# Performance work log

Hardware: AMD Instinct MI355X
Metric: run time of the kernel (lower is better)

Reference implementation:

```python
import jax, jax.numpy as jnp
import numpy as np

N_NODES = 131072
N_EDGES = 1048576
N_GRAPHS = 1024
EMB = 96
HID = 64
OUT = 3
NEG_SLOPE = 0.2  # PyG GATConv default leaky_relu slope


def setup_inputs() -> dict:
    key = jax.random.key(0)
    ks = jax.random.split(key, 8)
    x = jax.random.normal(ks[0], (N_NODES, EMB), dtype=jnp.float32)
    edge_index = jax.random.randint(ks[1], (2, N_EDGES), 0, N_NODES, dtype=jnp.int64)
    batch = jnp.sort(jax.random.randint(ks[2], (N_NODES,), 0, N_GRAPHS, dtype=jnp.int64))
    s = 1.0 / np.sqrt(EMB)
    W = jax.random.uniform(ks[3], (EMB, HID), jnp.float32, -s, s)       # GATConv lin (no bias)
    att_src = jax.random.uniform(ks[4], (HID,), jnp.float32, -s, s)     # a_src
    att_dst = jax.random.uniform(ks[5], (HID,), jnp.float32, -s, s)     # a_dst
    bias_gat = jnp.zeros((HID,), jnp.float32)
    sf = 1.0 / np.sqrt(HID)
    fc_w = jax.random.uniform(ks[6], (OUT, HID), jnp.float32, -sf, sf)
    fc_b = jax.random.uniform(ks[7], (OUT,), jnp.float32, -sf, sf)
    return {"x": x, "edge_index": edge_index, "batch": batch, "W": W,
            "att_src": att_src, "att_dst": att_dst, "bias_gat": bias_gat,
            "fc_w": fc_w, "fc_b": fc_b}


def _segment_softmax(logits, seg, num_segments):
    # numerically stable softmax over edges grouped by target node
    m = jax.ops.segment_max(logits, seg, num_segments=num_segments)
    e = jnp.exp(logits - m[seg])
    z = jax.ops.segment_sum(e, seg, num_segments=num_segments)
    return e / (z[seg] + 1e-16)


def reference(x, edge_index, batch, W, att_src, att_dst, bias_gat, fc_w, fc_b):
    N = x.shape[0]
    # PyG GATConv (heads=1): add self loops
    loop = jnp.arange(N, dtype=edge_index.dtype)
    src = jnp.concatenate([edge_index[0], loop])
    dst = jnp.concatenate([edge_index[1], loop])

    h = x @ W                                    # [N, HID]
    a_s = h @ att_src                            # [N]
    a_d = h @ att_dst                            # [N]
    logits = jax.nn.leaky_relu(a_s[src] + a_d[dst], NEG_SLOPE)  # [E]
    alpha = _segment_softmax(logits, dst, N)     # softmax over in-edges per target
    out = jax.ops.segment_sum(alpha[:, None] * h[src], dst, num_segments=N)
    out = out + bias_gat                         # [N, HID]

    # global_mean_pool over graphs
    sums = jax.ops.segment_sum(out, batch, num_segments=N_GRAPHS)
    cnt = jax.ops.segment_sum(jnp.ones((N,), out.dtype), batch, num_segments=N_GRAPHS)
    pooled = sums / jnp.maximum(cnt, 1.0)[:, None]  # [G, HID]

    logits_out = pooled @ fc_w.T + fc_b          # [G, OUT]
    return jax.nn.log_softmax(logits_out, axis=1)
```

## Files before the change

### kernel.cpp

```cpp
#include <hip/hip_runtime.h>
#include <hip/hip_fp16.h>

#define N_NODES 131072
#define N_EDGES 1048576
#define N_GRAPHS 1024
#define EMB 96
#define HID 64
#define CAP 32
#define NBKT 128
#define NCHUNK 1024
#define BCAP2 32

typedef _Float16 half8 __attribute__((ext_vector_type(8)));
typedef float float4v __attribute__((ext_vector_type(4)));

__global__ __launch_bounds__(256) void k_bucket(const int* __restrict__ src,
    const int* __restrict__ dst, int* __restrict__ ebuf, int* __restrict__ ccnt,
    const float* __restrict__ W, _Float16* __restrict__ Wt)
{
    int tid = threadIdx.x;
    int blk = blockIdx.x;
    __shared__ int bcnt[NBKT];
    if (tid < NBKT) bcnt[tid] = 0;
    if (blk < 24) {
        int t = blk * 256 + tid;
        Wt[(t & 63) * EMB + (t >> 6)] = (_Float16)W[t];
    }
    __syncthreads();
    int e0 = blk * 1024;
    #pragma unroll
    for (int i = 0; i < 4; ++i) {
        int e = e0 + i * 256 + tid;
        int sv = src[e], dv = dst[e];
        int b = dv >> 10;
        int r = atomicAdd(&bcnt[b], 1);
        if (r < BCAP2)
            ebuf[((size_t)b * NCHUNK + blk) * BCAP2 + r] = (sv << 10) | (dv & 1023);
    }
    __syncthreads();
    if (tid < NBKT) {
        int v = bcnt[tid];
        ccnt[tid * NCHUNK + blk] = v < BCAP2 ? v : BCAP2;
    }
}

__global__ __launch_bounds__(512, 4) void k_lin_place(
    const float* __restrict__ x, const _Float16* __restrict__ Wt,
    const float* __restrict__ att_src, const float* __restrict__ att_dst,
    __half* __restrict__ h, float* __restrict__ a_s, float* __restrict__ a_d,
    const int* __restrict__ ebuf, const int* __restrict__ ccnt,
    int* __restrict__ cnt, int* __restrict__ slots,
    float* __restrict__ pool, float* __restrict__ gcnt)
{
    int tid = threadIdx.x;
    __shared__ int cl[1024];
    __shared__ int cm[1024];

    if (blockIdx.x < NBKT) {
        int b = blockIdx.x;
        cl[tid] = 0; cl[tid + 512] = 0;
        cm[tid] = ccnt[b * NCHUNK + tid];
        cm[tid + 512] = ccnt[b * NCHUNK + 512 + tid];
        pool[b * 512 + tid] = 0.f;
        if (b == 0) { gcnt[tid] = 0.f; gcnt[tid + 512] = 0.f; }
        __syncthreads();
        int lane = tid & 63;
        int w = tid >> 6;
        int half = lane >> 5;
        int s32 = lane & 31;
        const int* eb = ebuf + (size_t)b * NCHUNK * BCAP2;
        int bbase = b << 10;
        for (int it0 = 0; it0 < 64; it0 += 8) {
            int e[8];
            #pragma unroll
            for (int k = 0; k < 8; ++k) {
                int c = w * 128 + (it0 + k) * 2 + half;
                e[k] = eb[c * BCAP2 + s32];
            }
            #pragma unroll
            for (int k = 0; k < 8; ++k) {
                int c = w * 128 + (it0 + k) * 2 + half;
                if (s32 < cm[c]) {
                    int local = e[k] & 1023;
                    int slot = atomicAdd(&cl[local], 1);
                    if (slot < CAP)
                        slots[(size_t)(bbase | local) * CAP + slot] = e[k] >> 10;
                }
            }
        }
        __syncthreads();
        cnt[b * 1024 + tid] = cl[tid];
        cnt[b * 1024 + 512 + tid] = cl[tid + 512];
    } else {
        int sub = blockIdx.x - NBKT;
        int lane = tid & 63;
        int w = tid >> 6;
        int m16 = lane & 15;
        int quad = lane >> 4;
        int rowbase = sub * 128 + w * 16;

        half8 bf[4][3];
        #pragma unroll
        for (int nt = 0; nt < 4; ++nt)
            #pragma unroll
            for (int kb = 0; kb < 3; ++kb)
                bf[nt][kb] = *(const half8*)(Wt + (nt * 16 + m16) * EMB
                                             + kb * 32 + quad * 8);

        float4v acc[4];
        #pragma unroll
        for (int nt = 0; nt < 4; ++nt)
            acc[nt] = (float4v){0.f, 0.f, 0.f, 0.f};

        const float* xrow = x + (size_t)(rowbase + m16) * EMB + quad * 8;
        #pragma unroll
        for (int kb = 0; kb < 3; ++kb) {
            float4 xa = *(const float4*)(xrow + kb * 32);
            float4 xb = *(const float4*)(xrow + kb * 32 + 4);
            half8 af;
            af[0] = (_Float16)xa.x; af[1] = (_Float16)xa.y;
            af[2] = (_Float16)xa.z; af[3] = (_Float16)xa.w;
            af[4] = (_Float16)xb.x; af[5] = (_Float16)xb.y;
            af[6] = (_Float16)xb.z; af[7] = (_Float16)xb.w;
            #pragma unroll
            for (int nt = 0; nt < 4; ++nt)
                acc[nt] = __builtin_amdgcn_mfma_f32_16x16x32_f16(
                    af, bf[nt][kb], acc[nt], 0, 0, 0);
        }

        float asv[4], adv[4];
        #pragma unroll
        for (int nt = 0; nt < 4; ++nt) {
            asv[nt] = att_src[nt * 16 + m16];
            adv[nt] = att_dst[nt * 16 + m16];
        }

        #pragma unroll
        for (int r = 0; r < 4; ++r) {
            int row = rowbase + quad * 4 + r;
            float ps = 0.f, pd = 0.f;
            #pragma unroll
            for (int nt = 0; nt < 4; ++nt) {
                float v = acc[nt][r];
                h[(size_t)row * HID + nt * 16 + m16] = __float2half(v);
                ps += v * asv[nt];
                pd += v * adv[nt];
            }
            #pragma unroll
            for (int off = 8; off >= 1; off >>= 1) {
                ps += __shfl_xor(ps, off, 64);
                pd += __shfl_xor(pd, off, 64);
            }
            if (m16 == 0) { a_s[row] = ps; a_d[row] = pd; }
        }
    }
}

__global__ __launch_bounds__(256, 6) void k_accum(const __half2* __restrict__ h2,
    const float* __restrict__ a_s, const float* __restrict__ a_d,
    const int* __restrict__ cnt, const int* __restrict__ slots,
    const float* __restrict__ bias, __half2* __restrict__ out)
{
    int tid = threadIdx.x;
    int lane = tid & 63;
    int sub = lane & 31;
    int gbase = lane & 32;
    int node = blockIdx.x * 8 + ((tid >> 6) << 1) + (gbase >> 5);

    int deg = cnt[node]; if (deg > CAP) deg = CAP;
    int s_j = node;
    if (sub < deg) s_j = slots[(size_t)node * CAP + sub];

    __half2 hv = h2[(size_t)node * 32 + sub];
    __half2 hg[16];
    #pragma unroll
    for (int k = 0; k < 16; ++k) {
        int i = __shfl(s_j, gbase + k, 64);
        hg[k] = h2[(size_t)i * 32 + sub];
    }
    float asg = a_s[s_j];
    float adi = a_d[node];
    float asi = a_s[node];

    float t = asg + adi;
    t = t > 0.f ? t : 0.2f * t;
    float w_j = (sub < deg) ? __expf(t) : 0.f;

    float t0 = asi + adi;
    t0 = t0 > 0.f ? t0 : 0.2f * t0;
    float w0 = __expf(t0);

    float z = w_j;
    #pragma unroll
    for (int off = 16; off >= 1; off >>= 1) z += __shfl_xor(z, off, 64);
    z += w0;

    float2 acc;
    acc.x = w0 * __half2float(hv.x);
    acc.y = w0 * __half2float(hv.y);
    #pragma unroll
    for (int k = 0; k < 16; ++k) {
        float wk = __shfl(w_j, gbase + k, 64);
        acc.x += wk * __half2float(hg[k].x);
        acc.y += wk * __half2float(hg[k].y);
    }

    for (int j0 = 16; j0 < deg; j0 += 8) {
        __half2 g2[8];
        #pragma unroll
        for (int k = 0; k < 8; ++k) {
            int i = __shfl(s_j, gbase + j0 + k, 64);
            g2[k] = h2[(size_t)i * 32 + sub];
        }
        #pragma unroll
        for (int k = 0; k < 8; ++k) {
            float wk = __shfl(w_j, gbase + j0 + k, 64);
            acc.x += wk * __half2float(g2[k].x);
            acc.y += wk * __half2float(g2[k].y);
        }
    }

    float inv = 1.f / (z + 1e-16f);
    float2 b2 = ((const float2*)bias)[sub];
    out[(size_t)node * 32 + sub] =
        __floats2half2_rn(acc.x * inv + b2.x, acc.y * inv + b2.y);
}

__global__ __launch_bounds__(256) void k_pool(const __half* __restrict__ out,
    const int* __restrict__ batch, float* __restrict__ pool,
    float* __restrict__ gcnt)
{
    int lane = threadIdx.x & 63;
    int wv = blockIdx.x * 4 + (threadIdx.x >> 6);
    int base = wv * 64;
    int bv = batch[base + lane];
    int g_cur = __shfl(bv, 0);
    float acc = 0.f;
    int run = 0;
    for (int c = 0; c < 8; ++c) {
        int n0 = base + c * 8;
        float v[8];
        #pragma unroll
        for (int k = 0; k < 8; ++k)
            v[k] = __half2float(out[(size_t)(n0 + k) * HID + lane]);
        int b0 = __shfl(bv, c * 8);
        int b7 = __shfl(bv, c * 8 + 7);
        if (b0 == b7) {
            if (b0 != g_cur) {
                atomicAdd(&pool[g_cur * HID + lane], acc);
                if (lane == 0) atomicAdd(&gcnt[g_cur], (float)run);
                acc = 0.f; run = 0; g_cur = b0;
            }
            acc += ((v[0] + v[1]) + (v[2] + v[3]))
                 + ((v[4] + v[5]) + (v[6] + v[7]));
            run += 8;
        } else {
            #pragma unroll
            for (int k = 0; k < 8; ++k) {
                int g = __shfl(bv, c * 8 + k);
                if (g != g_cur) {
                    atomicAdd(&pool[g_cur * HID + lane], acc);
                    if (lane == 0) atomicAdd(&gcnt[g_cur], (float)run);
                    acc = 0.f; run = 0; g_cur = g;
                }
                acc += v[k]; ++run;
            }
        }
    }
    atomicAdd(&pool[g_cur * HID + lane], acc);
    if (lane == 0) atomicAdd(&gcnt[g_cur], (float)run);
}

__global__ __launch_bounds__(256) void k_head(const float* __restrict__ pool,
    const float* __restrict__ gcnt, const float* __restrict__ fc_w,
    const float* __restrict__ fc_b, float* __restrict__ out)
{
    int tid = threadIdx.x;
    int lane = tid & 63;
    int g = blockIdx.x * 4 + (tid >> 6);
    float p = pool[g * HID + lane] / fmaxf(gcnt[g], 1.0f);
    float l0 = p * fc_w[0 * HID + lane];
    float l1 = p * fc_w[1 * HID + lane];
    float l2 = p * fc_w[2 * HID + lane];
    #pragma unroll
    for (int off = 32; off >= 1; off >>= 1) {
        l0 += __shfl_xor(l0, off, 64);
        l1 += __shfl_xor(l1, off, 64);
        l2 += __shfl_xor(l2, off, 64);
    }
    l0 += fc_b[0]; l1 += fc_b[1]; l2 += fc_b[2];
    float m = fmaxf(l0, fmaxf(l1, l2));
    float lse = m + logf(__expf(l0 - m) + __expf(l1 - m) + __expf(l2 - m));
    if (lane == 0) {
        out[g * 3 + 0] = l0 - lse;
        out[g * 3 + 1] = l1 - lse;
        out[g * 3 + 2] = l2 - lse;
    }
}

extern "C" void kernel_launch(void* const* d_in, const int* in_sizes, int n_in,
                              void* d_out, int out_size, void* d_ws, size_t ws_size,
                              hipStream_t stream)
{
    const float* x        = (const float*)d_in[0];
    const int*   ei       = (const int*)d_in[1];
    const int*   batch    = (const int*)d_in[2];
    const float* W        = (const float*)d_in[3];
    const float* att_src  = (const float*)d_in[4];
    const float* att_dst  = (const float*)d_in[5];
    const float* bias_gat = (const float*)d_in[6];
    const float* fc_w     = (const float*)d_in[7];
    const float* fc_b     = (const float*)d_in[8];
    float* out = (float*)d_out;

    char* ws = (char*)d_ws;
    size_t off = 0;
    auto alloc = [&](size_t bytes) {
        void* p = ws + off;
        off += (bytes + 255) & ~(size_t)255;
        return p;
    };
    __half* h    = (__half*)alloc((size_t)N_NODES * HID * 2);
    int*   slots = (int*)  alloc((size_t)N_NODES * CAP * 4);
    int*   cnt   = (int*)  alloc((size_t)N_NODES * 4);
    int*   ccnt  = (int*)  alloc((size_t)NCHUNK * NBKT * 4);
    float* a_s   = (float*)alloc((size_t)N_NODES * 4);
    float* a_d   = (float*)alloc((size_t)N_NODES * 4);
    float* pool  = (float*)alloc((size_t)N_GRAPHS * HID * 4);
    float* gcnt  = (float*)alloc((size_t)N_GRAPHS * 4);
    _Float16* Wt = (_Float16*)alloc((size_t)HID * EMB * 2);
    int*   ebuf  = (int*)alloc((size_t)NBKT * NCHUNK * BCAP2 * 4);
    __half* nout = (__half*)ebuf;

    const int* e_src = ei;
    const int* e_dst = ei + N_EDGES;

    k_bucket<<<NCHUNK, 256, 0, stream>>>(e_src, e_dst, ebuf, ccnt, W, Wt);
    k_lin_place<<<NBKT + 1024, 512, 0, stream>>>(x, Wt, att_src, att_dst,
                                                 h, a_s, a_d, ebuf, ccnt,
                                                 cnt, slots, pool, gcnt);
    k_accum <<<N_NODES / 8, 256, 0, stream>>>((const __half2*)h, a_s, a_d, cnt,
                                              slots, bias_gat, (__half2*)nout);
    k_pool  <<<N_NODES / 256, 256, 0, stream>>>(nout, batch, pool, gcnt);
    k_head  <<<N_GRAPHS / 4, 256, 0, stream>>>(pool, gcnt, fc_w, fc_b, out);
}
```

Baseline: 180.7 us.

## Replace two-pass bucketed CSR build with direct global-atomic slot placement

Drops the two-level bucketing scheme, where edges were first binned per 1024-node bucket and chunk and then placed into per-node slots with LDS atomics. Each edge now does a global atomicAdd on its destination's counter and writes its source directly into the slot array. A memset zeroes the counters and pooling buffers, and the linear kernel no longer shares a launch with placement. This saves a pass over the intermediate edge buffer and its extra traffic, at the cost of about a million scattered global atomics, which can contend and serialize.

```diff
diff --git a/kernel.cpp b/kernel.cpp
--- a/kernel.cpp
+++ b/kernel.cpp
@@ -6,153 +6,98 @@
 #define N_GRAPHS 1024
 #define EMB 96
 #define HID 64
+#define OUT 3
 #define CAP 32
-#define NBKT 128
-#define NCHUNK 1024
-#define BCAP2 32
 
 typedef _Float16 half8 __attribute__((ext_vector_type(8)));
 typedef float float4v __attribute__((ext_vector_type(4)));
 
-__global__ __launch_bounds__(256) void k_bucket(const int* __restrict__ src,
-    const int* __restrict__ dst, int* __restrict__ ebuf, int* __restrict__ ccnt,
+__global__ __launch_bounds__(256) void k_deg(const int* __restrict__ src,
+    const int* __restrict__ dst, int* __restrict__ cnt, int* __restrict__ slots,
     const float* __restrict__ W, _Float16* __restrict__ Wt)
 {
     int tid = threadIdx.x;
     int blk = blockIdx.x;
-    __shared__ int bcnt[NBKT];
-    if (tid < NBKT) bcnt[tid] = 0;
     if (blk < 24) {
         int t = blk * 256 + tid;
         Wt[(t & 63) * EMB + (t >> 6)] = (_Float16)W[t];
     }
-    __syncthreads();
     int e0 = blk * 1024;
     #pragma unroll
     for (int i = 0; i < 4; ++i) {
         int e = e0 + i * 256 + tid;
         int sv = src[e], dv = dst[e];
-        int b = dv >> 10;
-        int r = atomicAdd(&bcnt[b], 1);
-        if (r < BCAP2)
-            ebuf[((size_t)b * NCHUNK + blk) * BCAP2 + r] = (sv << 10) | (dv & 1023);
-    }
-    __syncthreads();
-    if (tid < NBKT) {
-        int v = bcnt[tid];
-        ccnt[tid * NCHUNK + blk] = v < BCAP2 ? v : BCAP2;
-    }
-}
-
-__global__ __launch_bounds__(512, 4) void k_lin_place(
+        int r = atomicAdd(&cnt[dv], 1);
+        if (r < CAP)
+            slots[(size_t)dv * CAP + r] = sv;
+    }
+}
+
+__global__ __launch_bounds__(512, 4) void k_lin(
     const float* __restrict__ x, const _Float16* __restrict__ Wt,
     const float* __restrict__ att_src, const float* __restrict__ att_dst,
-    __half* __restrict__ h, float* __restrict__ a_s, float* __restrict__ a_d,
-    const int* __restrict__ ebuf, const int* __restrict__ ccnt,
-    int* __restrict__ cnt, int* __restrict__ slots,
-    float* __restrict__ pool, float* __restrict__ gcnt)
-{
-    int tid = threadIdx.x;
-    __shared__ int cl[1024];
-    __shared__ int cm[1024];
-
-    if (blockIdx.x < NBKT) {
-        int b = blockIdx.x;
-        cl[tid] = 0; cl[tid + 512] = 0;
-        cm[tid] = ccnt[b * NCHUNK + tid];
-        cm[tid + 512] = ccnt[b * NCHUNK + 512 + tid];
-        pool[b * 512 + tid] = 0.f;
-        if (b == 0) { gcnt[tid] = 0.f; gcnt[tid + 512] = 0.f; }
-        __syncthreads();
-        int lane = tid & 63;
-        int w = tid >> 6;
-        int half = lane >> 5;
-        int s32 = lane & 31;
-        const int* eb = ebuf + (size_t)b * NCHUNK * BCAP2;
-        int bbase = b << 10;
-        for (int it0 = 0; it0 < 64; it0 += 8) {
-            int e[8];
-            #pragma unroll
-            for (int k = 0; k < 8; ++k) {
-                int c = w * 128 + (it0 + k) * 2 + half;
-                e[k] = eb[c * BCAP2 + s32];
-            }
-            #pragma unroll
-            for (int k = 0; k < 8; ++k) {
-                int c = w * 128 + (it0 + k) * 2 + half;
-                if (s32 < cm[c]) {
-                    int local = e[k] & 1023;
-                    int slot = atomicAdd(&cl[local], 1);
-                    if (slot < CAP)
-                        slots[(size_t)(bbase | local) * CAP + slot] = e[k] >> 10;
-                }
-            }
-        }
-        __syncthreads();
-        cnt[b * 1024 + tid] = cl[tid];
-        cnt[b * 1024 + 512 + tid] = cl[tid + 512];
-    } else {
-        int sub = blockIdx.x - NBKT;
-        int lane = tid & 63;
-        int w = tid >> 6;
-        int m16 = lane & 15;
-        int quad = lane >> 4;
-        int rowbase = sub * 128 + w * 16;
-
-        half8 bf[4][3];
+    __half* __restrict__ h, float* __restrict__ a_s, float* __restrict__ a_d)
+{
+    int tid = threadIdx.x;
+    int lane = tid & 63;
+    int w = tid >> 6;
+    int m16 = lane & 15;
+    int quad = lane >> 4;
+    int rowbase = blockIdx.x * 128 + w * 16;
+
+    half8 bf[4][3];
+    #pragma unroll
+    for (int nt = 0; nt < 4; ++nt)
+        #pragma unroll
+        for (int kb = 0; kb < 3; ++kb)
+            bf[nt][kb] = *(const half8*)(Wt + (nt * 16 + m16) * EMB
+                                         + kb * 32 + quad * 8);
+
+    float4v acc[4];
+    #pragma unroll
+    for (int nt = 0; nt < 4; ++nt)
+        acc[nt] = (float4v){0.f, 0.f, 0.f, 0.f};
+
+    const float* xrow = x + (size_t)(rowbase + m16) * EMB + quad * 8;
+    #pragma unroll
+    for (int kb = 0; kb < 3; ++kb) {
+        float4 xa = *(const float4*)(xrow + kb * 32);
+        float4 xb = *(const float4*)(xrow + kb * 32 + 4);
+        half8 af;
+        af[0] = (_Float16)xa.x; af[1] = (_Float16)xa.y;
+        af[2] = (_Float16)xa.z; af[3] = (_Float16)xa.w;
+        af[4] = (_Float16)xb.x; af[5] = (_Float16)xb.y;
+        af[6] = (_Float16)xb.z; af[7] = (_Float16)xb.w;
         #pragma unroll
         for (int nt = 0; nt < 4; ++nt)
-            #pragma unroll
-            for (int kb = 0; kb < 3; ++kb)
-                bf[nt][kb] = *(const half8*)(Wt + (nt * 16 + m16) * EMB
-                                             + kb * 32 + quad * 8);
-
-        float4v acc[4];
-        #pragma unroll
-        for (int nt = 0; nt < 4; ++nt)
-            acc[nt] = (float4v){0.f, 0.f, 0.f, 0.f};
-
-        const float* xrow = x + (size_t)(rowbase + m16) * EMB + quad * 8;
-        #pragma unroll
-        for (int kb = 0; kb < 3; ++kb) {
-            float4 xa = *(const float4*)(xrow + kb * 32);
-            float4 xb = *(const float4*)(xrow + kb * 32 + 4);
-            half8 af;
-            af[0] = (_Float16)xa.x; af[1] = (_Float16)xa.y;
-            af[2] = (_Float16)xa.z; af[3] = (_Float16)xa.w;
-            af[4] = (_Float16)xb.x; af[5] = (_Float16)xb.y;
-            af[6] = (_Float16)xb.z; af[7] = (_Float16)xb.w;
-            #pragma unroll
-            for (int nt = 0; nt < 4; ++nt)
-                acc[nt] = __builtin_amdgcn_mfma_f32_16x16x32_f16(
-                    af, bf[nt][kb], acc[nt], 0, 0, 0);
-        }
-
-        float asv[4], adv[4];
+            acc[nt] = __builtin_amdgcn_mfma_f32_16x16x32_f16(
+                af, bf[nt][kb], acc[nt], 0, 0, 0);
+    }
+
+    float asv[4], adv[4];
+    #pragma unroll
+    for (int nt = 0; nt < 4; ++nt) {
+        asv[nt] = att_src[nt * 16 + m16];
+        adv[nt] = att_dst[nt * 16 + m16];
+    }
+
+    #pragma unroll
+    for (int r = 0; r < 4; ++r) {
+        int row = rowbase + quad * 4 + r;
+        float ps = 0.f, pd = 0.f;
         #pragma unroll
         for (int nt = 0; nt < 4; ++nt) {
-            asv[nt] = att_src[nt * 16 + m16];
-            adv[nt] = att_dst[nt * 16 + m16];
-        }
-
-        #pragma unroll
-        for (int r = 0; r < 4; ++r) {
-            int row = rowbase + quad * 4 + r;
-            float ps = 0.f, pd = 0.f;
-            #pragma unroll
-            for (int nt = 0; nt < 4; ++nt) {
-                float v = acc[nt][r];
-                h[(size_t)row * HID + nt * 16 + m16] = __float2half(v);
-                ps += v * asv[nt];
-                pd += v * adv[nt];
-            }
-            #pragma unroll
-            for (int off = 8; off >= 1; off >>= 1) {
-                ps += __shfl_xor(ps, off, 64);
-                pd += __shfl_xor(pd, off, 64);
-            }
-            if (m16 == 0) { a_s[row] = ps; a_d[row] = pd; }
-        }
+            float v = acc[nt][r];
+            h[(size_t)row * HID + nt * 16 + m16] = __float2half(v);
+            ps += v * asv[nt];
+            pd += v * adv[nt];
+        }
+        #pragma unroll
+        for (int off = 8; off >= 1; off >>= 1) {
+            ps += __shfl_xor(ps, off, 64);
+            pd += __shfl_xor(pd, off, 64);
+        }
+        if (m16 == 0) { a_s[row] = ps; a_d[row] = pd; }
     }
 }
 
@@ -323,24 +268,23 @@
     __half* h    = (__half*)alloc((size_t)N_NODES * HID * 2);
     int*   slots = (int*)  alloc((size_t)N_NODES * CAP * 4);
     int*   cnt   = (int*)  alloc((size_t)N_NODES * 4);
-    int*   ccnt  = (int*)  alloc((size_t)NCHUNK * NBKT * 4);
+    float* pool  = (float*)alloc((size_t)N_GRAPHS * HID * 4);
+    float* gcnt  = (float*)alloc((size_t)N_GRAPHS * 4);
     float* a_s   = (float*)alloc((size_t)N_NODES * 4);
     float* a_d   = (float*)alloc((size_t)N_NODES * 4);
-    float* pool  = (float*)alloc((size_t)N_GRAPHS * HID * 4);
-    float* gcnt  = (float*)alloc((size_t)N_GRAPHS * 4);
     _Float16* Wt = (_Float16*)alloc((size_t)HID * EMB * 2);
-    int*   ebuf  = (int*)alloc((size_t)NBKT * NCHUNK * BCAP2 * 4);
-    __half* nout = (__half*)ebuf;
+    __half* nout = (__half*)alloc((size_t)N_NODES * HID * 2);
 
     const int* e_src = ei;
     const int* e_dst = ei + N_EDGES;
 
-    k_bucket<<<NCHUNK, 256, 0, stream>>>(e_src, e_dst, ebuf, ccnt, W, Wt);
-    k_lin_place<<<NBKT + 1024, 512, 0, stream>>>(x, Wt, att_src, att_dst,
-                                                 h, a_s, a_d, ebuf, ccnt,
-                                                 cnt, slots, pool, gcnt);
-    k_accum <<<N_NODES / 8, 256, 0, stream>>>((const __half2*)h, a_s, a_d, cnt,
-                                              slots, bias_gat, (__half2*)nout);
-    k_pool  <<<N_NODES / 256, 256, 0, stream>>>(nout, batch, pool, gcnt);
-    k_head  <<<N_GRAPHS / 4, 256, 0, stream>>>(pool, gcnt, fc_w, fc_b, out);
-}
+    hipMemsetAsync(cnt, 0, (size_t)N_NODES * 4 + (size_t)N_GRAPHS * HID * 4
+                           + (size_t)N_GRAPHS * 4, stream);
+    k_deg  <<<N_EDGES / 1024, 256, 0, stream>>>(e_src, e_dst, cnt, slots, W, Wt);
+    k_lin  <<<N_NODES / 128, 512, 0, stream>>>(x, Wt, att_src, att_dst,
+                                               h, a_s, a_d);
+    k_accum<<<N_NODES / 8, 256, 0, stream>>>((const __half2*)h, a_s, a_d, cnt,
+                                             slots, bias_gat, (__half2*)nout);
+    k_pool <<<N_NODES / 256, 256, 0, stream>>>(nout, batch, pool, gcnt);
+    k_head <<<N_GRAPHS / 4, 256, 0, stream>>>(pool, gcnt, fc_w, fc_b, out);
+}
```

After: 239.0 us. 1.32x slower.

## Split placement into its own kernel staging per-node slot lists in LDS

Applied to the files above, without the earlier changes.

Doubles the bucket count to 256 with 512 chunks of 2048 edges. The fused lin/place kernel is split into a k_place kernel and a separate k_lin kernel. k_place builds each bucket's 512 nodes × 32 slot lists in shared memory and writes them out with coalesced stores, replacing scattered global slot writes. The pool/gcnt zeroing moves to a hipMemsetAsync. In exchange the linear layer no longer overlaps with placement, there is an extra launch, and k_place uses 64KB+ of LDS per block, which limits occupancy.

```diff
diff --git a/kernel.cpp b/kernel.cpp
--- a/kernel.cpp
+++ b/kernel.cpp
@@ -6,9 +6,10 @@
 #define N_GRAPHS 1024
 #define EMB 96
 #define HID 64
+#define OUT 3
 #define CAP 32
-#define NBKT 128
-#define NCHUNK 1024
+#define NBKT 256
+#define NCHUNK 512
 #define BCAP2 32
 
 typedef _Float16 half8 __attribute__((ext_vector_type(8)));
@@ -27,15 +28,15 @@
         Wt[(t & 63) * EMB + (t >> 6)] = (_Float16)W[t];
     }
     __syncthreads();
-    int e0 = blk * 1024;
-    #pragma unroll
-    for (int i = 0; i < 4; ++i) {
+    int e0 = blk * 2048;
+    #pragma unroll
+    for (int i = 0; i < 8; ++i) {
         int e = e0 + i * 256 + tid;
         int sv = src[e], dv = dst[e];
-        int b = dv >> 10;
+        int b = dv >> 9;
         int r = atomicAdd(&bcnt[b], 1);
         if (r < BCAP2)
-            ebuf[((size_t)b * NCHUNK + blk) * BCAP2 + r] = (sv << 10) | (dv & 1023);
+            ebuf[((size_t)b * NCHUNK + blk) * BCAP2 + r] = (sv << 9) | (dv & 511);
     }
     __syncthreads();
     if (tid < NBKT) {
@@ -44,115 +45,109 @@
     }
 }
 
-__global__ __launch_bounds__(512, 4) void k_lin_place(
+__global__ __launch_bounds__(512) void k_place(const int* __restrict__ ebuf,
+    const int* __restrict__ ccnt, int* __restrict__ cnt, int* __restrict__ slots)
+{
+    int tid = threadIdx.x;
+    int b = blockIdx.x;
+    __shared__ int lists[512 * CAP];
+    __shared__ int cl[512];
+    __shared__ int cm[NCHUNK];
+    cl[tid] = 0;
+    cm[tid] = ccnt[b * NCHUNK + tid];
+    __syncthreads();
+    const int* eb = ebuf + (size_t)b * NCHUNK * BCAP2;
+    for (int it0 = 0; it0 < 32; it0 += 8) {
+        int e[8];
+        #pragma unroll
+        for (int k = 0; k < 8; ++k)
+            e[k] = eb[(it0 + k) * 512 + tid];
+        #pragma unroll
+        for (int k = 0; k < 8; ++k) {
+            int idx = (it0 + k) * 512 + tid;
+            int c = idx >> 5, s = idx & 31;
+            if (s < cm[c]) {
+                int local = e[k] & 511;
+                int slot = atomicAdd(&cl[local], 1);
+                if (slot < CAP)
+                    lists[local * CAP + slot] = e[k] >> 9;
+            }
+        }
+    }
+    __syncthreads();
+    int* sb = slots + (size_t)b * 512 * CAP;
+    #pragma unroll
+    for (int it = 0; it < 32; ++it)
+        sb[it * 512 + tid] = lists[it * 512 + tid];
+    int v = cl[tid];
+    cnt[b * 512 + tid] = v < CAP ? v : CAP;
+}
+
+__global__ __launch_bounds__(512, 4) void k_lin(
     const float* __restrict__ x, const _Float16* __restrict__ Wt,
     const float* __restrict__ att_src, const float* __restrict__ att_dst,
-    __half* __restrict__ h, float* __restrict__ a_s, float* __restrict__ a_d,
-    const int* __restrict__ ebuf, const int* __restrict__ ccnt,
-    int* __restrict__ cnt, int* __restrict__ slots,
-    float* __restrict__ pool, float* __restrict__ gcnt)
-{
-    int tid = threadIdx.x;
-    __shared__ int cl[1024];
-    __shared__ int cm[1024];
-
-    if (blockIdx.x < NBKT) {
-        int b = blockIdx.x;
-        cl[tid] = 0; cl[tid + 512] = 0;
-        cm[tid] = ccnt[b * NCHUNK + tid];
-        cm[tid + 512] = ccnt[b * NCHUNK + 512 + tid];
-        pool[b * 512 + tid] = 0.f;
-        if (b == 0) { gcnt[tid] = 0.f; gcnt[tid + 512] = 0.f; }
-        __syncthreads();
-        int lane = tid & 63;
-        int w = tid >> 6;
-        int half = lane >> 5;
-        int s32 = lane & 31;
-        const int* eb = ebuf + (size_t)b * NCHUNK * BCAP2;
-        int bbase = b << 10;
-        for (int it0 = 0; it0 < 64; it0 += 8) {
-            int e[8];
-            #pragma unroll
-            for (int k = 0; k < 8; ++k) {
-                int c = w * 128 + (it0 + k) * 2 + half;
-                e[k] = eb[c * BCAP2 + s32];
-            }
-            #pragma unroll
-            for (int k = 0; k < 8; ++k) {
-                int c = w * 128 + (it0 + k) * 2 + half;
-                if (s32 < cm[c]) {
-                    int local = e[k] & 1023;
-                    int slot = atomicAdd(&cl[local], 1);
-                    if (slot < CAP)
-                        slots[(size_t)(bbase | local) * CAP + slot] = e[k] >> 10;
-                }
-            }
-        }
-        __syncthreads();
-        cnt[b * 1024 + tid] = cl[tid];
-        cnt[b * 1024 + 512 + tid] = cl[tid + 512];
-    } else {
-        int sub = blockIdx.x - NBKT;
-        int lane = tid & 63;
-        int w = tid >> 6;
-        int m16 = lane & 15;
-        int quad = lane >> 4;
-        int rowbase = sub * 128 + w * 16;
-
-        half8 bf[4][3];
+    __half* __restrict__ h, float* __restrict__ a_s, float* __restrict__ a_d)
+{
+    int tid = threadIdx.x;
+    int lane = tid & 63;
+    int w = tid >> 6;
+    int m16 = lane & 15;
+    int quad = lane >> 4;
+    int rowbase = blockIdx.x * 128 + w * 16;
+
+    half8 bf[4][3];
+    #pragma unroll
+    for (int nt = 0; nt < 4; ++nt)
+        #pragma unroll
+        for (int kb = 0; kb < 3; ++kb)
+            bf[nt][kb] = *(const half8*)(Wt + (nt * 16 + m16) * EMB
+                                         + kb * 32 + quad * 8);
+
+    float4v acc[4];
+    #pragma unroll
+    for (int nt = 0; nt < 4; ++nt)
+        acc[nt] = (float4v){0.f, 0.f, 0.f, 0.f};
+
+    const float* xrow = x + (size_t)(rowbase + m16) * EMB + quad * 8;
+    #pragma unroll
+    for (int kb = 0; kb < 3; ++kb) {
+        float4 xa = *(const float4*)(xrow + kb * 32);
+        float4 xb = *(const float4*)(xrow + kb * 32 + 4);
+        half8 af;
+        af[0] = (_Float16)xa.x; af[1] = (_Float16)xa.y;
+        af[2] = (_Float16)xa.z; af[3] = (_Float16)xa.w;
+        af[4] = (_Float16)xb.x; af[5] = (_Float16)xb.y;
+        af[6] = (_Float16)xb.z; af[7] = (_Float16)xb.w;
         #pragma unroll
         for (int nt = 0; nt < 4; ++nt)
-            #pragma unroll
-            for (int kb = 0; kb < 3; ++kb)
-                bf[nt][kb] = *(const half8*)(Wt + (nt * 16 + m16) * EMB
-                                             + kb * 32 + quad * 8);
-
-        float4v acc[4];
-        #pragma unroll
-        for (int nt = 0; nt < 4; ++nt)
-            acc[nt] = (float4v){0.f, 0.f, 0.f, 0.f};
-
-        const float* xrow = x + (size_t)(rowbase + m16) * EMB + quad * 8;
-        #pragma unroll
-        for (int kb = 0; kb < 3; ++kb) {
-            float4 xa = *(const float4*)(xrow + kb * 32);
-            float4 xb = *(const float4*)(xrow + kb * 32 + 4);
-            half8 af;
-            af[0] = (_Float16)xa.x; af[1] = (_Float16)xa.y;
-            af[2] = (_Float16)xa.z; af[3] = (_Float16)xa.w;
-            af[4] = (_Float16)xb.x; af[5] = (_Float16)xb.y;
-            af[6] = (_Float16)xb.z; af[7] = (_Float16)xb.w;
-            #pragma unroll
-            for (int nt = 0; nt < 4; ++nt)
-                acc[nt] = __builtin_amdgcn_mfma_f32_16x16x32_f16(
-                    af, bf[nt][kb], acc[nt], 0, 0, 0);
-        }
-
-        float asv[4], adv[4];
+            acc[nt] = __builtin_amdgcn_mfma_f32_16x16x32_f16(
+                af, bf[nt][kb], acc[nt], 0, 0, 0);
+    }
+
+    float asv[4], adv[4];
+    #pragma unroll
+    for (int nt = 0; nt < 4; ++nt) {
+        asv[nt] = att_src[nt * 16 + m16];
+        adv[nt] = att_dst[nt * 16 + m16];
+    }
+
+    #pragma unroll
+    for (int r = 0; r < 4; ++r) {
+        int row = rowbase + quad * 4 + r;
+        float ps = 0.f, pd = 0.f;
         #pragma unroll
         for (int nt = 0; nt < 4; ++nt) {
-            asv[nt] = att_src[nt * 16 + m16];
-            adv[nt] = att_dst[nt * 16 + m16];
-        }
-
-        #pragma unroll
-        for (int r = 0; r < 4; ++r) {
-            int row = rowbase + quad * 4 + r;
-            float ps = 0.f, pd = 0.f;
-            #pragma unroll
-            for (int nt = 0; nt < 4; ++nt) {
-                float v = acc[nt][r];
-                h[(size_t)row * HID + nt * 16 + m16] = __float2half(v);
-                ps += v * asv[nt];
-                pd += v * adv[nt];
-            }
-            #pragma unroll
-            for (int off = 8; off >= 1; off >>= 1) {
-                ps += __shfl_xor(ps, off, 64);
-                pd += __shfl_xor(pd, off, 64);
-            }
-            if (m16 == 0) { a_s[row] = ps; a_d[row] = pd; }
-        }
+            float v = acc[nt][r];
+            h[(size_t)row * HID + nt * 16 + m16] = __float2half(v);
+            ps += v * asv[nt];
+            pd += v * adv[nt];
+        }
+        #pragma unroll
+        for (int off = 8; off >= 1; off >>= 1) {
+            ps += __shfl_xor(ps, off, 64);
+            pd += __shfl_xor(pd, off, 64);
+        }
+        if (m16 == 0) { a_s[row] = ps; a_d[row] = pd; }
     }
 }
 
@@ -323,11 +318,11 @@
     __half* h    = (__half*)alloc((size_t)N_NODES * HID * 2);
     int*   slots = (int*)  alloc((size_t)N_NODES * CAP * 4);
     int*   cnt   = (int*)  alloc((size_t)N_NODES * 4);
-    int*   ccnt  = (int*)  alloc((size_t)NCHUNK * NBKT * 4);
+    float* pool  = (float*)alloc((size_t)N_GRAPHS * HID * 4);
+    float* gcnt  = (float*)alloc((size_t)N_GRAPHS * 4);
     float* a_s   = (float*)alloc((size_t)N_NODES * 4);
     float* a_d   = (float*)alloc((size_t)N_NODES * 4);
-    float* pool  = (float*)alloc((size_t)N_GRAPHS * HID * 4);
-    float* gcnt  = (float*)alloc((size_t)N_GRAPHS * 4);
+    int*   ccnt  = (int*)  alloc((size_t)NBKT * NCHUNK * 4);
     _Float16* Wt = (_Float16*)alloc((size_t)HID * EMB * 2);
     int*   ebuf  = (int*)alloc((size_t)NBKT * NCHUNK * BCAP2 * 4);
     __half* nout = (__half*)ebuf;
@@ -335,10 +330,12 @@
     const int* e_src = ei;
     const int* e_dst = ei + N_EDGES;
 
+    hipMemsetAsync(pool, 0, (size_t)N_GRAPHS * HID * 4
+                            + (size_t)N_GRAPHS * 4, stream);
     k_bucket<<<NCHUNK, 256, 0, stream>>>(e_src, e_dst, ebuf, ccnt, W, Wt);
-    k_lin_place<<<NBKT + 1024, 512, 0, stream>>>(x, Wt, att_src, att_dst,
-                                                 h, a_s, a_d, ebuf, ccnt,
-                                                 cnt, slots, pool, gcnt);
+    k_place <<<NBKT, 512, 0, stream>>>(ebuf, ccnt, cnt, slots);
+    k_lin   <<<N_NODES / 128, 512, 0, stream>>>(x, Wt, att_src, att_dst,
+                                                h, a_s, a_d);
     k_accum <<<N_NODES / 8, 256, 0, stream>>>((const __half2*)h, a_s, a_d, cnt,
                                               slots, bias_gat, (__half2*)nout);
     k_pool  <<<N_NODES / 256, 256, 0, stream>>>(nout, batch, pool, gcnt);
```

New measurement: 174.5 us. -3.4%, faster.
